# Optimization experiments

Hardware: AMD Instinct MI355X
Metric: run time of the kernel (lower is better)

The kernel has to match this reference:

```python
import jax, jax.numpy as jnp
import numpy as np

H = 1024      # hidden_size
I = 2048      # expert intermediate_size (SwiGLU)
E = 8         # num_local_experts
B, S = 2, 4096
EPS = 1e-5
INIT = 0.02


def setup_inputs() -> dict:
    key = jax.random.key(0)
    ks = jax.random.split(key, 9)
    return {
        "hidden_states": jax.random.normal(ks[0], (B, S, H), jnp.float32),
        "ln_w": jnp.ones((H,), jnp.float32),
        "ln_b": jnp.zeros((H,), jnp.float32),
        "router_w": jax.random.normal(ks[1], (H, E), jnp.float32) * INIT,
        "gate_w": jax.random.normal(ks[2], (E, H, I), jnp.float32) * INIT,
        "up_w": jax.random.normal(ks[3], (E, H, I), jnp.float32) * INIT,
        "down_w": jax.random.normal(ks[4], (E, I, H), jnp.float32) * INIT,
        "sh_gate": jax.random.normal(ks[5], (H, I), jnp.float32) * INIT,
        "sh_up": jax.random.normal(ks[6], (H, I), jnp.float32) * INIT,
        "sh_down": jax.random.normal(ks[7], (I, H), jnp.float32) * INIT,
    }


def _layernorm(x, w, b):
    mu = jnp.mean(x, axis=-1, keepdims=True)
    var = jnp.mean(jnp.square(x - mu), axis=-1, keepdims=True)
    return (x - mu) * jax.lax.rsqrt(var + EPS) * w + b


def reference(hidden_states, ln_w, ln_b, router_w, gate_w, up_w, down_w,
              sh_gate, sh_up, sh_down):
    b, s, h = hidden_states.shape
    normed = _layernorm(hidden_states, ln_w, ln_b)
    xf = normed.reshape(-1, h)                       # [T, H]

    # Router: top-1 expert per token, sigmoid gating (Llama-4 style)
    logits = xf @ router_w                           # [T, E]
    top_idx = jnp.argmax(logits, axis=-1)            # [T]
    top_score = jax.nn.sigmoid(jnp.max(logits, axis=-1))  # [T]

    # Routed experts: scan over experts, mask+scale tokens assigned to each.
    def body(acc, ew):
        g, u, d, e = ew
        w = jnp.where(top_idx == e, top_score, 0.0)[:, None]  # [T, 1]
        xe = xf * w                                            # gate score applied to input
        hmid = jax.nn.silu(xe @ g) * (xe @ u)                  # [T, I]
        return acc + hmid @ d, None

    routed, _ = jax.lax.scan(
        body, jnp.zeros_like(xf), (gate_w, up_w, down_w, jnp.arange(E)))

    # Shared expert (dense SwiGLU) applied to all tokens
    shared = (jax.nn.silu(xf @ sh_gate) * (xf @ sh_up)) @ sh_down  # [T, H]

    moe_out = (routed + shared).reshape(b, s, h)
    return hidden_states + moe_out
```

## Files before the change

### kernel.cpp

```cpp
#include <hip/hip_runtime.h>

typedef unsigned short ushort_t;
typedef unsigned int uint_t;

#define T_TOK 8192
#define HDIM 1024
#define IDIM 2048
#define NEXP 8
#define RPAD_MAX 10240
#define TOTROWS (RPAD_MAX + T_TOK)

using f32x4 = __attribute__((ext_vector_type(4))) float;
using s16x8 = __attribute__((ext_vector_type(8))) short;

#define SBAR() do { asm volatile("" ::: "memory"); __builtin_amdgcn_s_barrier(); asm volatile("" ::: "memory"); } while (0)
#define VMW(n) asm volatile("s_waitcnt vmcnt(" #n ")" ::: "memory")
#define LGKM(n) do { asm volatile("s_waitcnt lgkmcnt(" #n ")" ::: "memory"); __builtin_amdgcn_sched_barrier(0); } while (0)
#define SCHB() __builtin_amdgcn_sched_barrier(0)

__device__ __forceinline__ float b2f(ushort_t h) {
    return __uint_as_float(((uint_t)h) << 16);
}
__device__ __forceinline__ ushort_t f2bf(float f) {
    uint_t u = __float_as_uint(f);
    uint_t r = (u + 0x7FFFu + ((u >> 16) & 1u)) >> 16;
    return (ushort_t)r;
}
__device__ __forceinline__ void gload16(const void* g, void* l) {
    __builtin_amdgcn_global_load_lds(
        (const __attribute__((address_space(1))) void*)g,
        (__attribute__((address_space(3))) void*)l, 16, 0, 0);
}
__device__ __forceinline__ void sbmap(int bid, int SBC, int NSB, int& rt, int& ct) {
    int x = bid & 7, j = bid >> 3;
    int r = j >> 5, pos = j & 31;
    int sb = r * 8 + x;
    int rem = NSB - r * 8;
    if (rem < 8) {
        int share = 8 / rem;
        int cap = 32 / share;
        sb = r * 8 + x / share;
        pos = (x % share) * cap + (pos % cap);
    }
    int sbr = sb / SBC, sbc = sb % SBC;
    rt = sbr * 4 + (pos >> 3);
    ct = sbc * 8 + (pos & 7);
}

__global__ void tcvt64(const float* __restrict__ gw, const float* __restrict__ shg,
                       const float* __restrict__ uw, const float* __restrict__ shu,
                       const float* __restrict__ dw, const float* __restrict__ shd,
                       ushort_t* __restrict__ gwt, ushort_t* __restrict__ uwt,
                       ushort_t* __restrict__ dwt) {
    __shared__ float tile[64][65];
    int z = blockIdx.z;
    const float* src;
    ushort_t* dst;
    int R, C, bx = blockIdx.x, by = blockIdx.y;
    if (z < 18) {
        int zz = z % 9;
        R = HDIM; C = IDIM;
        if (z < 9) { src = zz < 8 ? gw + (size_t)zz * HDIM * IDIM : shg; dst = gwt + (size_t)zz * IDIM * HDIM; }
        else       { src = zz < 8 ? uw + (size_t)zz * HDIM * IDIM : shu; dst = uwt + (size_t)zz * IDIM * HDIM; }
    } else {
        int zz = z - 18;
        R = IDIM; C = HDIM;
        src = zz < 8 ? dw + (size_t)zz * IDIM * HDIM : shd;
        dst = dwt + (size_t)zz * HDIM * IDIM;
        int t = bx; bx = by; by = t;
    }
    int c0 = bx * 64, r0 = by * 64;
    int tx = threadIdx.x, ty = threadIdx.y;
#pragma unroll
    for (int i = 0; i < 16; ++i)
        tile[ty + i * 4][tx] = src[(size_t)(r0 + ty + i * 4) * C + c0 + tx];
    __syncthreads();
    int tid = ty * 64 + tx;
    int rr = (tid & 15) * 4, cc0 = tid >> 4;
#pragma unroll
    for (int it = 0; it < 4; ++it) {
        int c = cc0 + it * 16;
        ushort4 v;
        v.x = f2bf(tile[rr + 0][c]);
        v.y = f2bf(tile[rr + 1][c]);
        v.z = f2bf(tile[rr + 2][c]);
        v.w = f2bf(tile[rr + 3][c]);
        *(ushort4*)&dst[(size_t)(c0 + c) * R + r0 + rr] = v;
    }
}

__global__ void ln_router(const float* __restrict__ x, const float* __restrict__ lnw,
                          const float* __restrict__ lnb, const float* __restrict__ rw,
                          ushort_t* __restrict__ normed, int* __restrict__ top_idx,
                          float* __restrict__ top_score, int* __restrict__ cnt) {
    int t = blockIdx.x, tid = threadIdx.x;
    const float* xr = x + (size_t)t * HDIM;
    float v[4];
    float s = 0.f, ss = 0.f;
#pragma unroll
    for (int i = 0; i < 4; i++) {
        v[i] = xr[tid + i * 256];
        s += v[i];
        ss += v[i] * v[i];
    }
#pragma unroll
    for (int o = 32; o; o >>= 1) {
        s += __shfl_down(s, o);
        ss += __shfl_down(ss, o);
    }
    __shared__ float rs_[4], rss_[4], stats[2];
    int wid = tid >> 6, lane = tid & 63;
    if (!lane) { rs_[wid] = s; rss_[wid] = ss; }
    __syncthreads();
    if (!tid) {
        float S = rs_[0] + rs_[1] + rs_[2] + rs_[3];
        float SS = rss_[0] + rss_[1] + rss_[2] + rss_[3];
        float mu = S * (1.f / HDIM);
        float var = SS * (1.f / HDIM) - mu * mu;
        stats[0] = mu;
        stats[1] = rsqrtf(var + 1e-5f);
    }
    __syncthreads();
    float mu = stats[0], rsg = stats[1];
    float lg[8] = {0, 0, 0, 0, 0, 0, 0, 0};
#pragma unroll
    for (int i = 0; i < 4; i++) {
        int h = tid + i * 256;
        float xn = (v[i] - mu) * rsg * lnw[h] + lnb[h];
        normed[(size_t)t * HDIM + h] = f2bf(xn);
        const float* rwh = rw + (size_t)h * NEXP;
#pragma unroll
        for (int e = 0; e < 8; e++) lg[e] += xn * rwh[e];
    }
#pragma unroll
    for (int o = 32; o; o >>= 1)
#pragma unroll
        for (int e = 0; e < 8; e++) lg[e] += __shfl_down(lg[e], o);
    __shared__ float lred[4][8];
    if (!lane)
#pragma unroll
        for (int e = 0; e < 8; e++) lred[wid][e] = lg[e];
    __syncthreads();
    if (!tid) {
        float best = -1e30f;
        int bi = 0;
#pragma unroll
        for (int e = 0; e < 8; e++) {
            float L = lred[0][e] + lred[1][e] + lred[2][e] + lred[3][e];
            if (L > best) { best = L; bi = e; }
        }
        top_idx[t] = bi;
        top_score[t] = 1.f / (1.f + __expf(-best));
        atomicAdd(&cnt[bi], 1);
    }
}

__global__ void scan_k(const int* __restrict__ cnt, int* __restrict__ pad_off,
                       int* __restrict__ fill) {
    if (threadIdx.x == 0) {
        int o = 0;
        for (int e = 0; e < NEXP; e++) {
            pad_off[e] = o;
            o += (cnt[e] + 255) & ~255;
        }
        pad_off[NEXP] = o;
    }
    if (threadIdx.x < NEXP) fill[threadIdx.x] = 0;
}

__global__ void scatter_k(const ushort_t* __restrict__ normed, const int* __restrict__ top_idx,
                          const float* __restrict__ top_score, const int* __restrict__ pad_off,
                          int* __restrict__ fill, int* __restrict__ order,
                          int* __restrict__ t2p, ushort_t* __restrict__ xs) {
    int t = blockIdx.x, tid = threadIdx.x;
    __shared__ int spos;
    if (!tid) {
        int e = top_idx[t];
        int p = pad_off[e] + atomicAdd(&fill[e], 1);
        order[p] = t;
        t2p[t] = p;
        spos = p;
    }
    __syncthreads();
    int pos = spos;
    float sc = top_score[t];
    const ushort4* src = (const ushort4*)(normed + (size_t)t * HDIM);
    ushort4* dst = (ushort4*)(xs + (size_t)pos * HDIM);
    ushort4 a = src[tid];
    a.x = f2bf(b2f(a.x) * sc);
    a.y = f2bf(b2f(a.y) * sc);
    a.z = f2bf(b2f(a.z) * sc);
    a.w = f2bf(b2f(a.w) * sc);
    dst[tid] = a;
}

__global__ __launch_bounds__(512, 2) void gemm1_k(
    const ushort_t* __restrict__ X, const ushort_t* __restrict__ Wg,
    const ushort_t* __restrict__ Wu, const int* __restrict__ pad_off,
    const int* __restrict__ t2p, ushort_t* __restrict__ hmid,
    ushort_t* __restrict__ hmidS) {
    __shared__ __align__(16) ushort_t lds[2 * 32768];
    const int CT = IDIM / 128;
    const int NH = HDIM / 64;
    int rt, ct;
    sbmap(blockIdx.x, CT / 8, (TOTROWS / 256 / 4) * (CT / 8), rt, ct);
    int row0 = rt * 256, col0 = ct * 128;
    int e;
    if (row0 >= RPAD_MAX) e = 8;
    else {
        if (row0 >= pad_off[NEXP]) return;
        e = 0;
        while (e < 7 && row0 >= pad_off[e + 1]) ++e;
    }
    const ushort_t* wgp = Wg + (size_t)e * IDIM * HDIM;
    const ushort_t* wup = Wu + (size_t)e * IDIM * HDIM;

    const int tid = threadIdx.x, l = tid & 63, w = tid >> 6;
    const int wm = w >> 2, wn = w & 3;
    const int lr = l & 15, lg4 = l >> 4;

    const ushort_t* sA[4];
#pragma unroll
    for (int j = 0; j < 4; ++j) {
        int gi = tid + j * 512, row = gi >> 3, kg = (gi & 7) ^ (row & 7);
        sA[j] = X + (size_t)(row0 + row) * HDIM + kg * 8;
    }
    const ushort_t *sBg[2], *sBu[2];
#pragma unroll
    for (int j = 0; j < 2; ++j) {
        int gi = tid + j * 512, row = gi >> 3, kg = (gi & 7) ^ (row & 7);
        sBg[j] = wgp + (size_t)(col0 + row) * HDIM + kg * 8;
        sBu[j] = wup + (size_t)(col0 + row) * HDIM + kg * 8;
    }
    const int sl0 = (lg4 ^ (lr & 7)) * 8, sl1 = ((4 + lg4) ^ (lr & 7)) * 8;
    const int aob = (wm * 128 + lr) * 64;
    const int bob = (wn * 32 + lr) * 64;

    f32x4 accg[8][2] = {};
    f32x4 accu[8][2] = {};

#define G1_STAGE(h) do { int ko = (h) * 64; int hb_ = ((h) & 1) * 32768;       \
        gload16(sA[0] + ko, &lds[hb_ + tid * 8]);                              \
        gload16(sA[1] + ko, &lds[hb_ + 4096 + tid * 8]);                       \
        gload16(sA[2] + ko, &lds[hb_ + 8192 + tid * 8]);                       \
        gload16(sA[3] + ko, &lds[hb_ + 12288 + tid * 8]);                      \
        gload16(sBg[0] + ko, &lds[hb_ + 16384 + tid * 8]);                     \
        gload16(sBg[1] + ko, &lds[hb_ + 20480 + tid * 8]);                     \
        gload16(sBu[0] + ko, &lds[hb_ + 24576 + tid * 8]);                     \
        gload16(sBu[1] + ko, &lds[hb_ + 28672 + tid * 8]); } while (0)

#define G1_PH(h, DOSTAGE) do {                                                 \
        const int hb = ((h) & 1) * 32768;                                      \
        if (DOSTAGE) G1_STAGE((h) + 1);                                        \
        s16x8 a0[8], a1[8], b0[4], b1[4];                                      \
        _Pragma("unroll")                                                      \
        for (int m = 0; m < 8; ++m) a0[m] = *(const s16x8*)&lds[hb + aob + m * 1024 + sl0]; \
        _Pragma("unroll")                                                      \
        for (int n = 0; n < 2; ++n) {                                          \
            b0[n] = *(const s16x8*)&lds[hb + 16384 + bob + n * 1024 + sl0];    \
            b0[2 + n] = *(const s16x8*)&lds[hb + 24576 + bob + n * 1024 + sl0]; \
        }                                                                      \
        SCHB();                                                                \
        _Pragma("unroll")                                                      \
        for (int m = 0; m < 8; ++m) a1[m] = *(const s16x8*)&lds[hb + aob + m * 1024 + sl1]; \
        _Pragma("unroll")                                                      \
        for (int n = 0; n < 2; ++n) {                                          \
            b1[n] = *(const s16x8*)&lds[hb + 16384 + bob + n * 1024 + sl1];    \
            b1[2 + n] = *(const s16x8*)&lds[hb + 24576 + bob + n * 1024 + sl1]; \
        }                                                                      \
        SCHB();                                                                \
        LGKM(12);                                                              \
        __builtin_amdgcn_s_setprio(1);                                         \
        _Pragma("unroll")                                                      \
        for (int m = 0; m < 8; ++m) {                                          \
            accg[m][0] = __builtin_amdgcn_mfma_f32_16x16x32_bf16(a0[m], b0[0], accg[m][0], 0, 0, 0); \
            accg[m][1] = __builtin_amdgcn_mfma_f32_16x16x32_bf16(a0[m], b0[1], accg[m][1], 0, 0, 0); \
            accu[m][0] = __builtin_amdgcn_mfma_f32_16x16x32_bf16(a0[m], b0[2], accu[m][0], 0, 0, 0); \
            accu[m][1] = __builtin_amdgcn_mfma_f32_16x16x32_bf16(a0[m], b0[3], accu[m][1], 0, 0, 0); \
        }                                                                      \
        __builtin_amdgcn_s_setprio(0);                                         \
        LGKM(0);                                                               \
        __builtin_amdgcn_s_setprio(1);                                         \
        _Pragma("unroll")                                                      \
        for (int m = 0; m < 8; ++m) {                                          \
            accg[m][0] = __builtin_amdgcn_mfma_f32_16x16x32_bf16(a1[m], b1[0], accg[m][0], 0, 0, 0); \
            accg[m][1] = __builtin_amdgcn_mfma_f32_16x16x32_bf16(a1[m], b1[1], accg[m][1], 0, 0, 0); \
            accu[m][0] = __builtin_amdgcn_mfma_f32_16x16x32_bf16(a1[m], b1[2], accu[m][0], 0, 0, 0); \
            accu[m][1] = __builtin_amdgcn_mfma_f32_16x16x32_bf16(a1[m], b1[3], accu[m][1], 0, 0, 0); \
        }                                                                      \
        __builtin_amdgcn_s_setprio(0);                                         \
        VMW(0);                                                                \
        SBAR();                                                                \
    } while (0)

    G1_STAGE(0);
    VMW(0);
    SBAR();
    for (int h = 0; h < NH - 1; ++h) G1_PH(h, 1);
    G1_PH(NH - 1, 0);

#pragma unroll
    for (int mf = 0; mf < 8; ++mf) {
        int row = row0 + wm * 128 + mf * 16 + lg4 * 4;
#pragma unroll
        for (int nf = 0; nf < 2; ++nf) {
            int col = col0 + wn * 32 + nf * 16 + lr;
#pragma unroll
            for (int rr = 0; rr < 4; ++rr) {
                float g = accg[mf][nf][rr], u = accu[mf][nf][rr];
                float val = g / (1.f + __expf(-g)) * u;
                if (e == 8) {
                    int t = row + rr - RPAD_MAX;
                    int p = t2p[t];
                    hmidS[(size_t)p * IDIM + col] = f2bf(val);
                } else {
                    hmid[(size_t)(row + rr) * IDIM + col] = f2bf(val);
                }
            }
        }
    }
#undef G1_STAGE
#undef G1_PH
}

__global__ __launch_bounds__(512, 2) void gemm2_k(
    const ushort_t* __restrict__ Hm, const ushort_t* __restrict__ HmS,
    const ushort_t* __restrict__ Wd, const int* __restrict__ pad_off,
    const int* __restrict__ order, const float* __restrict__ hs,
    float* __restrict__ out) {
    __shared__ __align__(16) ushort_t lds[2 * 32768];
    const int NH = IDIM / 64;
    int bid = blockIdx.x;
    int wg = (bid & 7) * 40 + (bid >> 3);
    int seg = wg >= 160 ? 1 : 0;
    int rem = wg - seg * 160;
    int rt = rem >> 2, ct = rem & 3;
    int row0 = rt * 256, col0 = ct * 256;
    if (row0 >= pad_off[NEXP]) return;
    const ushort_t* A;
    const ushort_t* wdp;
    if (seg) {
        A = HmS;
        wdp = Wd + (size_t)8 * HDIM * IDIM;
    } else {
        A = Hm;
        int e = 0;
        while (e < 7 && row0 >= pad_off[e + 1]) ++e;
        wdp = Wd + (size_t)e * HDIM * IDIM;
    }
    const int tid = threadIdx.x, l = tid & 63, w = tid >> 6;
    const int wm = w >> 2, wn = w & 3;
    const int lr = l & 15, lg4 = l >> 4;

    const ushort_t* sA[4];
    const ushort_t* sB[4];
#pragma unroll
    for (int j = 0; j < 4; ++j) {
        int gi = tid + j * 512, row = gi >> 3, kg = (gi & 7) ^ (row & 7);
        sA[j] = A + (size_t)(row0 + row) * IDIM + kg * 8;
        sB[j] = wdp + (size_t)(col0 + row) * IDIM + kg * 8;
    }
    const int sl0 = (lg4 ^ (lr & 7)) * 8, sl1 = ((4 + lg4) ^ (lr & 7)) * 8;
    const int aob = (wm * 128 + lr) * 64;
    const int bob = (wn * 64 + lr) * 64;

    f32x4 acc[8][4] = {};

#define G2_STAGE(h) do { int ko = (h) * 64; int hb_ = ((h) & 1) * 32768;       \
        gload16(sA[0] + ko, &lds[hb_ + tid * 8]);                              \
        gload16(sA[1] + ko, &lds[hb_ + 4096 + tid * 8]);                       \
        gload16(sA[2] + ko, &lds[hb_ + 8192 + tid * 8]);                       \
        gload16(sA[3] + ko, &lds[hb_ + 12288 + tid * 8]);                      \
        gload16(sB[0] + ko, &lds[hb_ + 16384 + tid * 8]);                      \
        gload16(sB[1] + ko, &lds[hb_ + 20480 + tid * 8]);                      \
        gload16(sB[2] + ko, &lds[hb_ + 24576 + tid * 8]);                      \
        gload16(sB[3] + ko, &lds[hb_ + 28672 + tid * 8]); } while (0)

#define G2_PH(h, DOSTAGE) do {                                                 \
        const int hb = ((h) & 1) * 32768;                                      \
        if (DOSTAGE) G2_STAGE((h) + 1);                                        \
        s16x8 a0[8], a1[8], b0[4], b1[4];                                      \
        _Pragma("unroll")                                                      \
        for (int m = 0; m < 8; ++m) a0[m] = *(const s16x8*)&lds[hb + aob + m * 1024 + sl0]; \
        _Pragma("unroll")                                                      \
        for (int n = 0; n < 4; ++n) b0[n] = *(const s16x8*)&lds[hb + 16384 + bob + n * 1024 + sl0]; \
        SCHB();                                                                \
        _Pragma("unroll")                                                      \
        for (int m = 0; m < 8; ++m) a1[m] = *(const s16x8*)&lds[hb + aob + m * 1024 + sl1]; \
        _Pragma("unroll")                                                      \
        for (int n = 0; n < 4; ++n) b1[n] = *(const s16x8*)&lds[hb + 16384 + bob + n * 1024 + sl1]; \
        SCHB();                                                                \
        LGKM(12);                                                              \
        __builtin_amdgcn_s_setprio(1);                                         \
        _Pragma("unroll")                                                      \
        for (int m = 0; m < 8; ++m)                                            \
            _Pragma("unroll")                                                  \
            for (int n = 0; n < 4; ++n)                                        \
                acc[m][n] = __builtin_amdgcn_mfma_f32_16x16x32_bf16(a0[m], b0[n], acc[m][n], 0, 0, 0); \
        __builtin_amdgcn_s_setprio(0);                                         \
        LGKM(0);                                                               \
        __builtin_amdgcn_s_setprio(1);                                         \
        _Pragma("unroll")                                                      \
        for (int m = 0; m < 8; ++m)                                            \
            _Pragma("unroll")                                                  \
            for (int n = 0; n < 4; ++n)                                        \
                acc[m][n] = __builtin_amdgcn_mfma_f32_16x16x32_bf16(a1[m], b1[n], acc[m][n], 0, 0, 0); \
        __builtin_amdgcn_s_setprio(0);                                         \
        VMW(0);                                                                \
        SBAR();                                                                \
    } while (0)

    G2_STAGE(0);
    VMW(0);
    SBAR();
    for (int h = 0; h < NH - 1; ++h) G2_PH(h, 1);
    G2_PH(NH - 1, 0);

#pragma unroll
    for (int mf = 0; mf < 8; ++mf) {
        int row = row0 + wm * 128 + mf * 16 + lg4 * 4;
#pragma unroll
        for (int rr = 0; rr < 4; ++rr) {
            int tok = order[row + rr];
            if (tok < 0) continue;
            size_t ob = (size_t)tok * HDIM;
#pragma unroll
            for (int nf = 0; nf < 4; ++nf) {
                int col = col0 + wn * 64 + nf * 16 + lr;
                float v = acc[mf][nf][rr];
                if (!seg) v += hs[ob + col];
                atomicAdd(&out[ob + col], v);
            }
        }
    }
#undef G2_STAGE
#undef G2_PH
}

extern "C" void kernel_launch(void* const* d_in, const int* in_sizes, int n_in,
                              void* d_out, int out_size, void* d_ws, size_t ws_size,
                              hipStream_t stream) {
    const float* hs = (const float*)d_in[0];
    const float* lnw = (const float*)d_in[1];
    const float* lnb = (const float*)d_in[2];
    const float* rw = (const float*)d_in[3];
    const float* gw = (const float*)d_in[4];
    const float* uw = (const float*)d_in[5];
    const float* dw = (const float*)d_in[6];
    const float* shg = (const float*)d_in[7];
    const float* shu = (const float*)d_in[8];
    const float* shd = (const float*)d_in[9];
    float* out = (float*)d_out;

    char* p = (char*)d_ws;
    auto alloc = [&](size_t bytes) {
        void* r = (void*)p;
        p += (bytes + 255) & ~(size_t)255;
        return r;
    };
    ushort_t* xsbuf = (ushort_t*)alloc((size_t)TOTROWS * HDIM * 2);
    ushort_t* hmid = (ushort_t*)alloc((size_t)RPAD_MAX * IDIM * 2);
    ushort_t* hmidS = (ushort_t*)alloc((size_t)RPAD_MAX * IDIM * 2);
    ushort_t* gwt = (ushort_t*)alloc((size_t)9 * IDIM * HDIM * 2);
    ushort_t* uwt = (ushort_t*)alloc((size_t)9 * IDIM * HDIM * 2);
    ushort_t* dwt = (ushort_t*)alloc((size_t)9 * HDIM * IDIM * 2);
    int* cnt = (int*)alloc(NEXP * 4);
    int* pad_off = (int*)alloc((NEXP + 1) * 4);
    int* fill = (int*)alloc(NEXP * 4);
    int* top_idx = (int*)alloc(T_TOK * 4);
    float* top_sc = (float*)alloc(T_TOK * 4);
    int* order = (int*)alloc(RPAD_MAX * 4);
    int* t2p = (int*)alloc(T_TOK * 4);

    ushort_t* normed = xsbuf + (size_t)RPAD_MAX * HDIM;

    hipMemsetAsync(cnt, 0, NEXP * 4, stream);
    hipMemsetAsync(order, 0xFF, RPAD_MAX * 4, stream);
    hipMemsetAsync(xsbuf, 0, (size_t)RPAD_MAX * HDIM * 2, stream);
    hipMemsetAsync(out, 0, (size_t)T_TOK * HDIM * 4, stream);

    tcvt64<<<dim3(IDIM / 64, HDIM / 64, 27), dim3(64, 4), 0, stream>>>(
        gw, shg, uw, shu, dw, shd, gwt, uwt, dwt);

    ln_router<<<T_TOK, 256, 0, stream>>>(hs, lnw, lnb, rw, normed, top_idx, top_sc, cnt);
    scan_k<<<1, 64, 0, stream>>>(cnt, pad_off, fill);
    scatter_k<<<T_TOK, 256, 0, stream>>>(normed, top_idx, top_sc, pad_off, fill, order, t2p, xsbuf);

    {
        int RT = TOTROWS / 256, CT = IDIM / 128;
        gemm1_k<<<RT * CT, 512, 0, stream>>>(xsbuf, gwt, uwt, pad_off, t2p, hmid, hmidS);
    }
    gemm2_k<<<320, 512, 0, stream>>>(hmid, hmidS, dwt, pad_off, order, hs, out);
}
```

Baseline: 702.3 us.

## Split down-projection into routed and shared launches, replacing atomics with plain stores

The second GEMM is split into two templated launches. The routed pass writes each token's output with a plain store, since every token appears exactly once in the routed rows. The shared pass then read-modify-writes the residual plus the shared expert output. This removes the float atomics, the output memset and the t2p indirection, and gemm1 now writes shared rows contiguously into one hmid buffer. The next-stage global prefetch is also moved after the LDS fragment reads in both GEMMs, and the cost is serializing the two down-projection passes instead of running them in one grid.

```diff
diff --git a/kernel.cpp b/kernel.cpp
--- a/kernel.cpp
+++ b/kernel.cpp
@@ -171,14 +171,13 @@
 __global__ void scatter_k(const ushort_t* __restrict__ normed, const int* __restrict__ top_idx,
                           const float* __restrict__ top_score, const int* __restrict__ pad_off,
                           int* __restrict__ fill, int* __restrict__ order,
-                          int* __restrict__ t2p, ushort_t* __restrict__ xs) {
+                          ushort_t* __restrict__ xs) {
     int t = blockIdx.x, tid = threadIdx.x;
     __shared__ int spos;
     if (!tid) {
         int e = top_idx[t];
         int p = pad_off[e] + atomicAdd(&fill[e], 1);
         order[p] = t;
-        t2p[t] = p;
         spos = p;
     }
     __syncthreads();
@@ -197,8 +196,7 @@
 __global__ __launch_bounds__(512, 2) void gemm1_k(
     const ushort_t* __restrict__ X, const ushort_t* __restrict__ Wg,
     const ushort_t* __restrict__ Wu, const int* __restrict__ pad_off,
-    const int* __restrict__ t2p, ushort_t* __restrict__ hmid,
-    ushort_t* __restrict__ hmidS) {
+    ushort_t* __restrict__ hmid) {
     __shared__ __align__(16) ushort_t lds[2 * 32768];
     const int CT = IDIM / 128;
     const int NH = HDIM / 64;
@@ -251,7 +249,6 @@
 
 #define G1_PH(h, DOSTAGE) do {                                                 \
         const int hb = ((h) & 1) * 32768;                                      \
-        if (DOSTAGE) G1_STAGE((h) + 1);                                        \
         s16x8 a0[8], a1[8], b0[4], b1[4];                                      \
         _Pragma("unroll")                                                      \
         for (int m = 0; m < 8; ++m) a0[m] = *(const s16x8*)&lds[hb + aob + m * 1024 + sl0]; \
@@ -269,6 +266,7 @@
             b1[2 + n] = *(const s16x8*)&lds[hb + 24576 + bob + n * 1024 + sl1]; \
         }                                                                      \
         SCHB();                                                                \
+        if (DOSTAGE) G1_STAGE((h) + 1);                                        \
         LGKM(12);                                                              \
         __builtin_amdgcn_s_setprio(1);                                         \
         _Pragma("unroll")                                                      \
@@ -309,13 +307,7 @@
             for (int rr = 0; rr < 4; ++rr) {
                 float g = accg[mf][nf][rr], u = accu[mf][nf][rr];
                 float val = g / (1.f + __expf(-g)) * u;
-                if (e == 8) {
-                    int t = row + rr - RPAD_MAX;
-                    int p = t2p[t];
-                    hmidS[(size_t)p * IDIM + col] = f2bf(val);
-                } else {
-                    hmid[(size_t)(row + rr) * IDIM + col] = f2bf(val);
-                }
+                hmid[(size_t)(row + rr) * IDIM + col] = f2bf(val);
             }
         }
     }
@@ -323,27 +315,26 @@
 #undef G1_PH
 }
 
+template <int SHARED>
 __global__ __launch_bounds__(512, 2) void gemm2_k(
-    const ushort_t* __restrict__ Hm, const ushort_t* __restrict__ HmS,
-    const ushort_t* __restrict__ Wd, const int* __restrict__ pad_off,
-    const int* __restrict__ order, const float* __restrict__ hs,
-    float* __restrict__ out) {
+    const ushort_t* __restrict__ Hm, const ushort_t* __restrict__ Wd,
+    const int* __restrict__ pad_off, const int* __restrict__ order,
+    const float* __restrict__ hs, float* __restrict__ out, int RT) {
     __shared__ __align__(16) ushort_t lds[2 * 32768];
+    const int CT = 4;
     const int NH = IDIM / 64;
+    int nwg = RT * CT;
     int bid = blockIdx.x;
-    int wg = (bid & 7) * 40 + (bid >> 3);
-    int seg = wg >= 160 ? 1 : 0;
-    int rem = wg - seg * 160;
-    int rt = rem >> 2, ct = rem & 3;
+    int q = nwg >> 3, r = nwg & 7;
+    int xcd = bid & 7, idx = bid >> 3;
+    int wg = (xcd < r ? xcd * (q + 1) : r * (q + 1) + (xcd - r) * q) + idx;
+    int rt = wg >> 2, ct = wg & 3;
     int row0 = rt * 256, col0 = ct * 256;
-    if (row0 >= pad_off[NEXP]) return;
-    const ushort_t* A;
     const ushort_t* wdp;
-    if (seg) {
-        A = HmS;
+    if (SHARED) {
         wdp = Wd + (size_t)8 * HDIM * IDIM;
     } else {
-        A = Hm;
+        if (row0 >= pad_off[NEXP]) return;
         int e = 0;
         while (e < 7 && row0 >= pad_off[e + 1]) ++e;
         wdp = Wd + (size_t)e * HDIM * IDIM;
@@ -357,7 +348,7 @@
 #pragma unroll
     for (int j = 0; j < 4; ++j) {
         int gi = tid + j * 512, row = gi >> 3, kg = (gi & 7) ^ (row & 7);
-        sA[j] = A + (size_t)(row0 + row) * IDIM + kg * 8;
+        sA[j] = Hm + (size_t)(row0 + row) * IDIM + kg * 8;
         sB[j] = wdp + (size_t)(col0 + row) * IDIM + kg * 8;
     }
     const int sl0 = (lg4 ^ (lr & 7)) * 8, sl1 = ((4 + lg4) ^ (lr & 7)) * 8;
@@ -378,7 +369,6 @@
 
 #define G2_PH(h, DOSTAGE) do {                                                 \
         const int hb = ((h) & 1) * 32768;                                      \
-        if (DOSTAGE) G2_STAGE((h) + 1);                                        \
         s16x8 a0[8], a1[8], b0[4], b1[4];                                      \
         _Pragma("unroll")                                                      \
         for (int m = 0; m < 8; ++m) a0[m] = *(const s16x8*)&lds[hb + aob + m * 1024 + sl0]; \
@@ -390,6 +380,7 @@
         _Pragma("unroll")                                                      \
         for (int n = 0; n < 4; ++n) b1[n] = *(const s16x8*)&lds[hb + 16384 + bob + n * 1024 + sl1]; \
         SCHB();                                                                \
+        if (DOSTAGE) G2_STAGE((h) + 1);                                        \
         LGKM(12);                                                              \
         __builtin_amdgcn_s_setprio(1);                                         \
         _Pragma("unroll")                                                      \
@@ -421,15 +412,16 @@
         int row = row0 + wm * 128 + mf * 16 + lg4 * 4;
 #pragma unroll
         for (int rr = 0; rr < 4; ++rr) {
-            int tok = order[row + rr];
-            if (tok < 0) continue;
+            int rw_ = row + rr;
+            int tok;
+            if (SHARED) tok = rw_;
+            else { tok = order[rw_]; if (tok < 0) continue; }
             size_t ob = (size_t)tok * HDIM;
 #pragma unroll
             for (int nf = 0; nf < 4; ++nf) {
                 int col = col0 + wn * 64 + nf * 16 + lr;
-                float v = acc[mf][nf][rr];
-                if (!seg) v += hs[ob + col];
-                atomicAdd(&out[ob + col], v);
+                if (SHARED) out[ob + col] += hs[ob + col] + acc[mf][nf][rr];
+                else        out[ob + col] = acc[mf][nf][rr];
             }
         }
     }
@@ -459,8 +451,7 @@
         return r;
     };
     ushort_t* xsbuf = (ushort_t*)alloc((size_t)TOTROWS * HDIM * 2);
-    ushort_t* hmid = (ushort_t*)alloc((size_t)RPAD_MAX * IDIM * 2);
-    ushort_t* hmidS = (ushort_t*)alloc((size_t)RPAD_MAX * IDIM * 2);
+    ushort_t* hmid = (ushort_t*)alloc((size_t)TOTROWS * IDIM * 2);
     ushort_t* gwt = (ushort_t*)alloc((size_t)9 * IDIM * HDIM * 2);
     ushort_t* uwt = (ushort_t*)alloc((size_t)9 * IDIM * HDIM * 2);
     ushort_t* dwt = (ushort_t*)alloc((size_t)9 * HDIM * IDIM * 2);
@@ -470,25 +461,32 @@
     int* top_idx = (int*)alloc(T_TOK * 4);
     float* top_sc = (float*)alloc(T_TOK * 4);
     int* order = (int*)alloc(RPAD_MAX * 4);
-    int* t2p = (int*)alloc(T_TOK * 4);
 
     ushort_t* normed = xsbuf + (size_t)RPAD_MAX * HDIM;
 
     hipMemsetAsync(cnt, 0, NEXP * 4, stream);
     hipMemsetAsync(order, 0xFF, RPAD_MAX * 4, stream);
     hipMemsetAsync(xsbuf, 0, (size_t)RPAD_MAX * HDIM * 2, stream);
-    hipMemsetAsync(out, 0, (size_t)T_TOK * HDIM * 4, stream);
 
     tcvt64<<<dim3(IDIM / 64, HDIM / 64, 27), dim3(64, 4), 0, stream>>>(
         gw, shg, uw, shu, dw, shd, gwt, uwt, dwt);
 
     ln_router<<<T_TOK, 256, 0, stream>>>(hs, lnw, lnb, rw, normed, top_idx, top_sc, cnt);
     scan_k<<<1, 64, 0, stream>>>(cnt, pad_off, fill);
-    scatter_k<<<T_TOK, 256, 0, stream>>>(normed, top_idx, top_sc, pad_off, fill, order, t2p, xsbuf);
+    scatter_k<<<T_TOK, 256, 0, stream>>>(normed, top_idx, top_sc, pad_off, fill, order, xsbuf);
 
     {
         int RT = TOTROWS / 256, CT = IDIM / 128;
-        gemm1_k<<<RT * CT, 512, 0, stream>>>(xsbuf, gwt, uwt, pad_off, t2p, hmid, hmidS);
-    }
-    gemm2_k<<<320, 512, 0, stream>>>(hmid, hmidS, dwt, pad_off, order, hs, out);
-}
+        gemm1_k<<<RT * CT, 512, 0, stream>>>(xsbuf, gwt, uwt, pad_off, hmid);
+    }
+    {
+        int RT = RPAD_MAX / 256;
+        gemm2_k<0><<<RT * 4, 512, 0, stream>>>(
+            hmid, dwt, pad_off, order, hs, out, RT);
+    }
+    {
+        int RT = T_TOK / 256;
+        gemm2_k<1><<<RT * 4, 512, 0, stream>>>(
+            hmid + (size_t)RPAD_MAX * IDIM, dwt, pad_off, order, hs, out, RT);
+    }
+}
```

Result: faster. 562.8 us, median of 2 (-19.9%).
